# Optimization experiments

Measured on AMD Instinct MI355X. Metric: run time of the kernel, lower is better.

## Reference

```python
import jax, jax.numpy as jnp
import numpy as np

B, L, C, K, NLEV, VOCAB, OUT = 32, 1024, 512, 2, 4, 128, 11


def setup_inputs() -> dict:
    key = jax.random.key(0)
    ks = jax.random.split(key, 8)
    x = jax.random.randint(ks[0], (B, L), 0, VOCAB, dtype=jnp.int32)
    mask = jax.random.randint(ks[1], (B, L), 0, 2).astype(jnp.bool_)
    emb = jax.random.uniform(ks[2], (VOCAB, C), minval=-0.5, maxval=0.5, dtype=jnp.float32)
    w1 = jax.random.normal(ks[3], (NLEV, C, C, K), dtype=jnp.float32) * 0.02
    b1 = jnp.zeros((NLEV, C), dtype=jnp.float32)
    w2 = jax.random.normal(ks[4], (NLEV, C, C, K), dtype=jnp.float32) * 0.02
    b2 = jnp.zeros((NLEV, C), dtype=jnp.float32)
    dec_w = jax.random.uniform(ks[5], (OUT, C), minval=-0.5, maxval=0.5, dtype=jnp.float32)
    dec_b = jnp.zeros((OUT,), dtype=jnp.float32)
    return dict(x=x, mask=mask, emb=emb, w1=w1, b1=b1, w2=w2, b2=b2, dec_w=dec_w, dec_b=dec_b)


def _causal_conv(h, w, b, dilation):
    # h: [B, C, L], w: [Cout, Cin, K]; left-pad (K-1)*d == conv+chomp in TCN
    pad = (w.shape[-1] - 1) * dilation
    out = jax.lax.conv_general_dilated(
        h, w, window_strides=(1,), padding=[(pad, 0)],
        rhs_dilation=(dilation,), dimension_numbers=("NCH", "OIH", "NCH"))
    return out + b[None, :, None]


def reference(x, mask, emb, w1, b1, w2, b2, dec_w, dec_b):
    h = emb[x].transpose(0, 2, 1)  # [B, C, L]
    for i in range(NLEV):  # fixed small number of TCN levels
        d = 2 ** i
        res = h
        h = jax.nn.relu(_causal_conv(h, w1[i], b1[i], d))
        h = jax.nn.relu(_causal_conv(h, w2[i], b2[i], d))
        h = jax.nn.relu(h + res)  # residual (in==out channels -> identity shortcut)
    y = jnp.einsum("bcl,oc->blo", h, dec_w) + dec_b  # [B, L, OUT]
    # mask-gather: original keeps only mask-true positions; zero others (jit-safe)
    return y * mask[..., None].astype(y.dtype)
```

## Files before the change

kernel.cpp:

```cpp
#include <hip/hip_runtime.h>
#include <stdint.h>

#define BB 32
#define LL 1024
#define CC 512
#define NN (BB * LL)
#define NLEVS 4
#define OUTD 11
#define LPAD 8
#define LROWS (LL + LPAD)

typedef __attribute__((ext_vector_type(8))) short bf16x8;
typedef __attribute__((ext_vector_type(4))) float f32x4;

static __device__ __forceinline__ unsigned short f2bf(float f) {
    union { float f; uint32_t u; } v; v.f = f;
    uint32_t u = v.u;
    uint32_t r = (u + 0x7fffu + ((u >> 16) & 1u)) >> 16;
    return (unsigned short)r;
}
static __device__ __forceinline__ float bf2f(unsigned short h) {
    union { uint32_t u; float f; } v; v.u = ((uint32_t)h) << 16;
    return v.f;
}

static __device__ __forceinline__ void llds16(const unsigned short* g, unsigned short* l) {
    __builtin_amdgcn_global_load_lds(
        (const __attribute__((address_space(1))) unsigned int*)g,
        (__attribute__((address_space(3))) unsigned int*)l, 16, 0, 0);
}

__global__ __launch_bounds__(256) void prep_kernel(
    const int* __restrict__ x, const float* __restrict__ emb,
    const float* __restrict__ w1, const float* __restrict__ w2,
    const float* __restrict__ dw,
    unsigned short* __restrict__ Hb0, unsigned short* __restrict__ Hb1,
    unsigned short* __restrict__ WpT, unsigned short* __restrict__ dwp)
{
    int b = blockIdx.x;
    if (b < 16384) {
        int e = b * 256 + threadIdx.x;
        int cv = e >> 19;
        int r = e & 524287;
        int j = r >> 12;
        int co = (r >> 3) & 511;
        int h = r & 7;
        int kidx = j * 8 + h;
        int k = (kidx < 512) ? 1 : 0;
        int ci = kidx & 511;
        int lvl = cv >> 1;
        const float* w = (cv & 1) ? w2 : w1;
        WpT[e] = f2bf(w[(((size_t)(lvl * 512 + co) * 512) + ci) * 2 + k]);
    } else if (b < 24576) {
        int t = (b - 16384) * 256 + threadIdx.x;
        int n = t >> 6;
        int c8 = (t & 63) * 8;
        int idx = x[n];
        const float* src = emb + (size_t)idx * CC + c8;
        float4 v0 = *(const float4*)src;
        float4 v1 = *(const float4*)(src + 4);
        ushort4 a, bb;
        a.x = f2bf(v0.x); a.y = f2bf(v0.y); a.z = f2bf(v0.z); a.w = f2bf(v0.w);
        bb.x = f2bf(v1.x); bb.y = f2bf(v1.y); bb.z = f2bf(v1.z); bb.w = f2bf(v1.w);
        int prow = (n >> 10) * LROWS + LPAD + (n & (LL - 1));
        unsigned short* dst = Hb0 + (size_t)prow * CC + c8;
        *(ushort4*)dst = a;
        *(ushort4*)(dst + 4) = bb;
    } else if (b < 24704) {
        int t = (b - 24576) * 256 + threadIdx.x;
        unsigned short* base = (t >> 14) ? Hb1 : Hb0;
        int rem = t & 16383;
        int p = rem >> 9;
        int q = rem & 511;
        size_t off = (size_t)p * (LROWS * CC) + (size_t)q * 8;
        *(uint4*)(base + off) = (uint4){0u, 0u, 0u, 0u};
    } else {
        int e = (b - 24704) * 256 + threadIdx.x;
        int jb = e >> 7;
        int o = (e >> 3) & 15;
        int j = e & 7;
        dwp[e] = f2bf((o < OUTD) ? dw[o * CC + jb * 8 + j] : 0.f);
    }
}

#define BUFH (17 * 512)
template <bool HAS_RES>
__global__ __launch_bounds__(256, 4) void conv_gemm(
    const unsigned short* __restrict__ Ain, const unsigned short* __restrict__ WpT,
    const float* __restrict__ bias, const unsigned short* __restrict__ resB,
    unsigned short* __restrict__ OutB, int d)
{
    __shared__ unsigned short sA[2 * BUFH];

    const int tid = threadIdx.x;
    const int wave = tid >> 6, lane = tid & 63;

    const int bid = blockIdx.x;
    const int xcd = bid & 7;
    const int local = bid >> 3;
    const int cb = local >> 5;
    const int nb = xcd + 8 * (local & 31);
    const int co0 = cb * 128;
    const int n0 = nb * 128;

    const int rbase = (n0 >> 10) * LROWS + LPAD + (n0 & (LL - 1));
    const int wm = (wave >> 1) * 64;
    const int wn = (wave & 1) * 64;
    const int lm = lane & 15, quad = lane >> 4;

    const int r8 = lane >> 3;
    const int c8 = lane & 7;

    f32x4 acc[4][4];
#pragma unroll
    for (int i = 0; i < 4; ++i)
#pragma unroll
        for (int j = 0; j < 4; ++j) acc[i][j] = (f32x4){0.f, 0.f, 0.f, 0.f};

    auto stage = [&](int it, int buf) {
        const int ci0 = it * 64;
        const unsigned short* gA =
            Ain + (size_t)(rbase - 8 + r8) * CC + ci0 + (c8 ^ r8) * 8;
        unsigned short* lbase = sA + buf * BUFH;
        for (int seg = wave; seg < 17; seg += 4)
            llds16(gA + (size_t)seg * 8 * CC, lbase + seg * 512);
    };

    stage(0, 0);
    __syncthreads();

    for (int it = 0; it < 8; ++it) {
        if (it < 7) stage(it + 1, (it + 1) & 1);
        const unsigned short* buf = sA + (it & 1) * BUFH;
        const int jb0 = it * 8;

        auto loadA = [&](int s, bf16x8* af) {
            const int t = s >> 1, ks = s & 1;
            const int shift = t ? d : 0;
            const int rowoff = 8 - shift + wm;
            const int key = (8 - shift + lm) & 7;
            const int cpos = ((ks * 4 + quad) ^ key);
#pragma unroll
            for (int mt = 0; mt < 4; ++mt)
                af[mt] = *(const bf16x8*)&buf[(rowoff + mt * 16 + lm) * 64 + cpos * 8];
        };
        auto loadB = [&](int s, bf16x8* bf) {
            const int t = s >> 1, ks = s & 1;
            const int jb = t * 64 + jb0 + ks * 4 + quad;
            const unsigned short* bbase = WpT + ((size_t)jb * 512 + co0 + wn + lm) * 8;
#pragma unroll
            for (int nt = 0; nt < 4; ++nt)
                bf[nt] = *(const bf16x8*)(bbase + (size_t)nt * 16 * 8);
        };

        bf16x8 afc[4], bfc[4], afn[4], bfn[4];
        loadA(0, afc);
        loadB(0, bfc);
#pragma unroll
        for (int s = 0; s < 4; ++s) {
            if (s < 3) { loadA(s + 1, afn); loadB(s + 1, bfn); }
#pragma unroll
            for (int mt = 0; mt < 4; ++mt)
#pragma unroll
                for (int nt = 0; nt < 4; ++nt)
                    acc[mt][nt] = __builtin_amdgcn_mfma_f32_16x16x32_bf16(
                        afc[mt], bfc[nt], acc[mt][nt], 0, 0, 0);
            if (s < 3) {
#pragma unroll
                for (int q2 = 0; q2 < 4; ++q2) { afc[q2] = afn[q2]; bfc[q2] = bfn[q2]; }
            }
        }
        __syncthreads();
    }

    float bv[4];
#pragma unroll
    for (int nt = 0; nt < 4; ++nt) bv[nt] = bias[co0 + wn + nt * 16 + lm];

#pragma unroll
    for (int mt = 0; mt < 4; ++mt) {
        int prow0 = rbase + wm + mt * 16 + quad * 4;
#pragma unroll
        for (int nt = 0; nt < 4; ++nt) {
            int co = co0 + wn + nt * 16 + lm;
#pragma unroll
            for (int r = 0; r < 4; ++r) {
                size_t off = (size_t)(prow0 + r) * CC + co;
                float v = acc[mt][nt][r] + bv[nt];
                v = fmaxf(v, 0.f);
                if (HAS_RES) {
                    v += bf2f(resB[off]);
                    v = fmaxf(v, 0.f);
                }
                OutB[off] = f2bf(v);
            }
        }
    }
}

__global__ __launch_bounds__(256) void decode_kernel(
    const unsigned short* __restrict__ H, const unsigned short* __restrict__ dwp,
    const float* __restrict__ db, const int* __restrict__ mask,
    float* __restrict__ out)
{
    const int wave = threadIdx.x >> 6, lane = threadIdx.x & 63;
    const int lm = lane & 15, quad = lane >> 4;
    const int n0 = blockIdx.x * 64 + wave * 16;
    const int prow = ((n0 + lm) >> 10) * LROWS + LPAD + ((n0 + lm) & (LL - 1));

    f32x4 acc = (f32x4){0.f, 0.f, 0.f, 0.f};
#pragma unroll
    for (int ks = 0; ks < 16; ++ks) {
        bf16x8 af = *(const bf16x8*)&H[(size_t)prow * CC + ks * 32 + quad * 8];
        bf16x8 bf = *(const bf16x8*)&dwp[((size_t)(ks * 4 + quad) * 16 + lm) * 8];
        acc = __builtin_amdgcn_mfma_f32_16x16x32_bf16(af, bf, acc, 0, 0, 0);
    }

    if (lm < OUTD) {
        float bo = db[lm];
#pragma unroll
        for (int r = 0; r < 4; ++r) {
            int n = n0 + quad * 4 + r;
            float v = (mask[n] != 0) ? (acc[r] + bo) : 0.f;
            out[(size_t)n * OUTD + lm] = v;
        }
    }
}

extern "C" void kernel_launch(void* const* d_in, const int* in_sizes, int n_in,
                              void* d_out, int out_size, void* d_ws, size_t ws_size,
                              hipStream_t stream)
{
    const int* x = (const int*)d_in[0];
    const int* mask = (const int*)d_in[1];
    const float* emb = (const float*)d_in[2];
    const float* w1 = (const float*)d_in[3];
    const float* b1 = (const float*)d_in[4];
    const float* w2 = (const float*)d_in[5];
    const float* b2 = (const float*)d_in[6];
    const float* dw = (const float*)d_in[7];
    const float* db = (const float*)d_in[8];
    float* out = (float*)d_out;

    char* ws = (char*)d_ws;
    const size_t HBB = (size_t)BB * LROWS * CC * 2;
    unsigned short* Hb0 = (unsigned short*)ws;
    unsigned short* Hb1 = (unsigned short*)(ws + HBB);
    unsigned short* WpT = (unsigned short*)(ws + 2 * HBB);
    unsigned short* dwp = (unsigned short*)(ws + 2 * HBB + (size_t)NLEVS * 2 * CC * 1024 * 2);

    prep_kernel<<<24736, 256, 0, stream>>>(x, emb, w1, w2, dw, Hb0, Hb1, WpT, dwp);

    const int grid = (CC / 128) * (NN / 128);
    for (int i = 0; i < NLEVS; ++i) {
        int d = 1 << i;
        const unsigned short* W1 = WpT + (size_t)(i * 2 + 0) * CC * 1024;
        const unsigned short* W2 = WpT + (size_t)(i * 2 + 1) * CC * 1024;
        conv_gemm<false><<<grid, 256, 0, stream>>>(Hb0, W1, b1 + i * CC, nullptr, Hb1, d);
        conv_gemm<true><<<grid, 256, 0, stream>>>(Hb1, W2, b2 + i * CC, Hb0, Hb0, d);
    }
    decode_kernel<<<NN / 64, 256, 0, stream>>>(Hb0, dwp, db, mask, out);
}
```

Baseline: 392.2 us.

## Replace block barriers with per-stage LDS ready/done counters and partial waitcnt

Replaces the __syncthreads at each K-iteration with shared-memory atomic counters: each wave signals when its async global-to-LDS loads for a stage have landed (via a partial vmcnt wait that leaves the next stage's loads in flight) and when it has finished reading a buffer. Waves spin with s_sleep on these counters, so prefetch of stage it+1 can stay outstanding while stage it is consumed. The intent is to remove full-block barrier stalls and keep the double buffer overlapped. In exchange it adds LDS atomics and spin loops, and relies on hand-encoded waitcnt immediates matching the per-wave load counts, which is fragile.

Result: faster. 379.8 us (-3.2%).

```diff
diff --git a/kernel.cpp b/kernel.cpp
--- a/kernel.cpp
+++ b/kernel.cpp
@@ -91,6 +91,8 @@
     unsigned short* __restrict__ OutB, int d)
 {
     __shared__ unsigned short sA[2 * BUFH];
+    __shared__ int s_ready[8];
+    __shared__ int s_done[8];
 
     const int tid = threadIdx.x;
     const int wave = tid >> 6, lane = tid & 63;
@@ -111,26 +113,43 @@
     const int r8 = lane >> 3;
     const int c8 = lane & 7;
 
+    if (tid < 8) { s_ready[tid] = 0; s_done[tid] = 0; }
+    __syncthreads();
+
     f32x4 acc[4][4];
 #pragma unroll
     for (int i = 0; i < 4; ++i)
 #pragma unroll
         for (int j = 0; j < 4; ++j) acc[i][j] = (f32x4){0.f, 0.f, 0.f, 0.f};
 
-    auto stage = [&](int it, int buf) {
-        const int ci0 = it * 64;
+    auto issue = [&](int it) {
         const unsigned short* gA =
-            Ain + (size_t)(rbase - 8 + r8) * CC + ci0 + (c8 ^ r8) * 8;
-        unsigned short* lbase = sA + buf * BUFH;
+            Ain + (size_t)(rbase - 8 + r8) * CC + it * 64 + (c8 ^ r8) * 8;
+        unsigned short* lbase = sA + (it & 1) * BUFH;
         for (int seg = wave; seg < 17; seg += 4)
             llds16(gA + (size_t)seg * 8 * CC, lbase + seg * 512);
     };
-
-    stage(0, 0);
-    __syncthreads();
+    auto spin4 = [&](int* p) {
+        volatile int* vp = (volatile int*)p;
+        while (*vp < 4) __builtin_amdgcn_s_sleep(1);
+    };
+
+    issue(0);
 
     for (int it = 0; it < 8; ++it) {
-        if (it < 7) stage(it + 1, (it + 1) & 1);
+        if (it < 7) {
+            if (it >= 1) spin4(&s_done[it - 1]);
+            issue(it + 1);
+            if (wave == 0) __builtin_amdgcn_s_waitcnt(0xF75);
+            else           __builtin_amdgcn_s_waitcnt(0xF74);
+        } else {
+            __builtin_amdgcn_s_waitcnt(0xF70);
+        }
+        __asm__ volatile("" ::: "memory");
+        if (lane == 0) atomicAdd(&s_ready[it], 1);
+        spin4(&s_ready[it]);
+        __asm__ volatile("" ::: "memory");
+
         const unsigned short* buf = sA + (it & 1) * BUFH;
         const int jb0 = it * 8;
 
@@ -170,7 +189,9 @@
                 for (int q2 = 0; q2 < 4; ++q2) { afc[q2] = afn[q2]; bfc[q2] = bfn[q2]; }
             }
         }
-        __syncthreads();
+
+        __asm__ volatile("" ::: "memory");
+        if (lane == 0) atomicAdd(&s_done[it], 1);
     }
 
     float bv[4];
```

## Give each wave a private LDS A-tile and drop block barriers

Applied to the files above, without the earlier changes.

Each wave now stages its own 72-row A slice into a private double-buffered LDS region and waits on vmcnt instead of block-wide __syncthreads. All B fragments for an iteration are loaded into registers up front, and launch bounds drop from 4 to 2 blocks per CU. The goal is to remove barrier stalls and let waves run independently. The cost is redundant halo loads (9 segments per wave versus 17 shared), more LDS and registers, and reliance on hand-coded waitcnt encodings that must match the exact count of outstanding loads.

Measured after the change: 431.0 us. 9.9% more time.

```diff
diff --git a/kernel.cpp b/kernel.cpp
--- a/kernel.cpp
+++ b/kernel.cpp
@@ -83,14 +83,14 @@
     }
 }
 
-#define BUFH (17 * 512)
+#define WBUF (72 * 64)
 template <bool HAS_RES>
-__global__ __launch_bounds__(256, 4) void conv_gemm(
+__global__ __launch_bounds__(256, 2) void conv_gemm(
     const unsigned short* __restrict__ Ain, const unsigned short* __restrict__ WpT,
     const float* __restrict__ bias, const unsigned short* __restrict__ resB,
     unsigned short* __restrict__ OutB, int d)
 {
-    __shared__ unsigned short sA[2 * BUFH];
+    __shared__ unsigned short sA[4][2 * WBUF];
 
     const int tid = threadIdx.x;
     const int wave = tid >> 6, lane = tid & 63;
@@ -111,66 +111,76 @@
     const int r8 = lane >> 3;
     const int c8 = lane & 7;
 
+    const unsigned short* gAw =
+        Ain + (size_t)(rbase + wm - 8 + r8) * CC + (c8 ^ r8) * 8;
+    unsigned short* const slot0 = sA[wave];
+    unsigned short* const slot1 = sA[wave] + WBUF;
+
+    auto issueA = [&](int it) {
+        const unsigned short* g = gAw + it * 64;
+        unsigned short* l = (it & 1) ? slot1 : slot0;
+#pragma unroll
+        for (int seg = 0; seg < 9; ++seg)
+            llds16(g + (size_t)seg * 8 * CC, l + seg * 512);
+    };
+
     f32x4 acc[4][4];
 #pragma unroll
     for (int i = 0; i < 4; ++i)
 #pragma unroll
         for (int j = 0; j < 4; ++j) acc[i][j] = (f32x4){0.f, 0.f, 0.f, 0.f};
 
-    auto stage = [&](int it, int buf) {
-        const int ci0 = it * 64;
-        const unsigned short* gA =
-            Ain + (size_t)(rbase - 8 + r8) * CC + ci0 + (c8 ^ r8) * 8;
-        unsigned short* lbase = sA + buf * BUFH;
-        for (int seg = wave; seg < 17; seg += 4)
-            llds16(gA + (size_t)seg * 8 * CC, lbase + seg * 512);
-    };
-
-    stage(0, 0);
-    __syncthreads();
+    issueA(0);
 
     for (int it = 0; it < 8; ++it) {
-        if (it < 7) stage(it + 1, (it + 1) & 1);
-        const unsigned short* buf = sA + (it & 1) * BUFH;
-        const int jb0 = it * 8;
+        bf16x8 ball[4][4];
+#pragma unroll
+        for (int s = 0; s < 4; ++s) {
+            const int t = s >> 1, ks = s & 1;
+            const int jb = t * 64 + it * 8 + ks * 4 + quad;
+            const unsigned short* bbase = WpT + ((size_t)jb * 512 + co0 + wn + lm) * 8;
+#pragma unroll
+            for (int nt = 0; nt < 4; ++nt)
+                ball[s][nt] = *(const bf16x8*)(bbase + (size_t)nt * 16 * 8);
+        }
+
+        if (it < 7) {
+            issueA(it + 1);
+            __builtin_amdgcn_s_waitcnt(0xF79);
+        } else {
+            __builtin_amdgcn_s_waitcnt(0xF70);
+        }
+        __asm__ volatile("" ::: "memory");
+
+        const unsigned short* buf = (it & 1) ? slot1 : slot0;
 
         auto loadA = [&](int s, bf16x8* af) {
             const int t = s >> 1, ks = s & 1;
             const int shift = t ? d : 0;
-            const int rowoff = 8 - shift + wm;
+            const int rowoff = 8 - shift;
             const int key = (8 - shift + lm) & 7;
             const int cpos = ((ks * 4 + quad) ^ key);
 #pragma unroll
             for (int mt = 0; mt < 4; ++mt)
                 af[mt] = *(const bf16x8*)&buf[(rowoff + mt * 16 + lm) * 64 + cpos * 8];
         };
-        auto loadB = [&](int s, bf16x8* bf) {
-            const int t = s >> 1, ks = s & 1;
-            const int jb = t * 64 + jb0 + ks * 4 + quad;
-            const unsigned short* bbase = WpT + ((size_t)jb * 512 + co0 + wn + lm) * 8;
-#pragma unroll
-            for (int nt = 0; nt < 4; ++nt)
-                bf[nt] = *(const bf16x8*)(bbase + (size_t)nt * 16 * 8);
-        };
-
-        bf16x8 afc[4], bfc[4], afn[4], bfn[4];
+
+        bf16x8 afc[4], afn[4];
         loadA(0, afc);
-        loadB(0, bfc);
 #pragma unroll
         for (int s = 0; s < 4; ++s) {
-            if (s < 3) { loadA(s + 1, afn); loadB(s + 1, bfn); }
+            if (s < 3) loadA(s + 1, afn);
 #pragma unroll
             for (int mt = 0; mt < 4; ++mt)
 #pragma unroll
                 for (int nt = 0; nt < 4; ++nt)
                     acc[mt][nt] = __builtin_amdgcn_mfma_f32_16x16x32_bf16(
-                        afc[mt], bfc[nt], acc[mt][nt], 0, 0, 0);
+                        afc[mt], ball[s][nt], acc[mt][nt], 0, 0, 0);
             if (s < 3) {
 #pragma unroll
-                for (int q2 = 0; q2 < 4; ++q2) { afc[q2] = afn[q2]; bfc[q2] = bfn[q2]; }
+                for (int q2 = 0; q2 < 4; ++q2) afc[q2] = afn[q2];
             }
         }
-        __syncthreads();
     }
 
     float bv[4];
```
